# Kernel tuning notes

Hardware: AMD Instinct MI355X
Metric: run time of the kernel (lower is better)

## Reference

```python
import jax, jax.numpy as jnp
import numpy as np

B, S, HID = 4, 1024, 4096
NH, NKV, HD = 32, 8, 128
FF = 11008
EPS = 1e-6
THETA = 10000.0


def rms_norm(x, w, eps=EPS):
    v = jnp.mean(jnp.square(x), axis=-1, keepdims=True)
    return x * jax.lax.rsqrt(v + eps) * w


def rotate_half(x):
    x1, x2 = jnp.split(x, 2, axis=-1)
    return jnp.concatenate([-x2, x1], axis=-1)


def rope_cos_sin(position_ids, head_dim=HD, theta=THETA):
    inv_freq = 1.0 / (theta ** (jnp.arange(0, head_dim, 2, dtype=jnp.float32) / head_dim))
    freqs = position_ids.astype(jnp.float32)[..., None] * inv_freq  # [B,S,HD/2]
    emb = jnp.concatenate([freqs, freqs], axis=-1)  # [B,S,HD]
    return jnp.cos(emb)[:, None, :, :], jnp.sin(emb)[:, None, :, :]  # [B,1,S,HD]


def setup_inputs() -> dict:
    key = jax.random.key(0)
    ks = jax.random.split(key, 9)
    sc = 0.02
    pos = jnp.tile(jnp.arange(S, dtype=jnp.int64 if jax.config.jax_enable_x64 else jnp.int32)[None, :], (B, 1))
    causal = jnp.tril(jnp.ones((S, S), dtype=bool))
    mask = jnp.where(causal, 0.0, -1e9).astype(jnp.float32)[None, None]  # [1,1,S,S]
    return {
        "hidden_states": jax.random.normal(ks[0], (B * S, HID), jnp.float32),
        "position_ids": pos,
        "attn_mask": mask,
        "Wq": jax.random.normal(ks[1], (HID, NH * HD), jnp.float32) * sc,
        "Wk": jax.random.normal(ks[2], (HID, NKV * HD), jnp.float32) * sc,
        "Wv": jax.random.normal(ks[3], (HID, NKV * HD), jnp.float32) * sc,
        "Wo": jax.random.normal(ks[4], (NH * HD, HID), jnp.float32) * sc,
        "ln1_w": jnp.ones((HID,), jnp.float32),
        "ln2_w": jnp.ones((HID,), jnp.float32),
        "w_gate": jax.random.normal(ks[5], (HID, FF), jnp.float32) * sc,
        "w_up": jax.random.normal(ks[6], (HID, FF), jnp.float32) * sc,
        "w_down": jax.random.normal(ks[7], (FF, HID), jnp.float32) * sc,
    }


def reference(hidden_states, position_ids, attn_mask, Wq, Wk, Wv, Wo, ln1_w, ln2_w, w_gate, w_up, w_down):
    residual = hidden_states
    h = rms_norm(hidden_states, ln1_w)

    # QKV projections on flat tokens, then reshape per train partition
    q = (h @ Wq).reshape(B, S, NH, HD).transpose(0, 2, 1, 3)     # [B,NH,S,HD]
    k = (h @ Wk).reshape(B, S, NKV, HD).transpose(0, 2, 1, 3)    # [B,NKV,S,HD]
    v = (h @ Wv).reshape(B, S, NKV, HD).transpose(0, 2, 1, 3)

    cos, sin = rope_cos_sin(position_ids)
    q = q * cos + rotate_half(q) * sin
    k = k * cos + rotate_half(k) * sin

    n_rep = NH // NKV
    k = jnp.repeat(k, n_rep, axis=1)  # [B,NH,S,HD]
    v = jnp.repeat(v, n_rep, axis=1)

    scores = jnp.einsum('bhqd,bhkd->bhqk', q, k) / np.sqrt(HD)
    scores = scores + attn_mask
    # softmax in fp32 as in the source
    probs = jax.nn.softmax(scores.astype(jnp.float32), axis=-1).astype(q.dtype)
    attn = jnp.einsum('bhqk,bhkd->bhqd', probs, v)               # [B,NH,S,HD]
    attn = attn.transpose(0, 2, 1, 3).reshape(B * S, NH * HD)
    h = attn @ Wo

    h = residual + h
    residual = h
    h2 = rms_norm(h, ln2_w)
    mlp = (jax.nn.silu(h2 @ w_gate) * (h2 @ w_up)) @ w_down
    return residual + mlp
```

## Files before the change

kernel.cpp:

```cpp
#include <hip/hip_runtime.h>

#define DEVINL __device__ __forceinline__

typedef unsigned short u16;
typedef __attribute__((ext_vector_type(8))) short bf16x8;
typedef __attribute__((ext_vector_type(4))) float f32x4;
typedef __attribute__((ext_vector_type(4))) unsigned short u16x4;


DEVINL float bf2f(u16 u) { union { unsigned i; float f; } x; x.i = ((unsigned)u) << 16; return x.f; }
DEVINL u16 f2bf(float f) {
  union { float f; unsigned i; } x; x.f = f;
  unsigned r = x.i + 0x7fffu + ((x.i >> 16) & 1u);
  return (u16)(r >> 16);
}

DEVINL void async16(u16* lds, const u16* g) {
  __builtin_amdgcn_global_load_lds((const __attribute__((address_space(1))) unsigned*)g,
                                   (__attribute__((address_space(3))) unsigned*)lds, 16, 0, 0);
}

__global__ __launch_bounds__(256) void conv_t(const float* __restrict__ in,
                                              u16* __restrict__ out, int K, int N) {
  __shared__ float tile[64][65];
  int k0 = blockIdx.y << 6, n0 = blockIdx.x << 6;
  int t = threadIdx.x;
  int r = t >> 4, c4 = (t & 15) << 2;
  #pragma unroll
  for (int it = 0; it < 4; it++) {
    int row = r + it*16;
    f32x4 v = *(const f32x4*)(in + (size_t)(k0 + row)*N + n0 + c4);
    tile[row][c4+0] = v[0]; tile[row][c4+1] = v[1];
    tile[row][c4+2] = v[2]; tile[row][c4+3] = v[3];
  }
  __syncthreads();
  #pragma unroll
  for (int it = 0; it < 4; it++) {
    int nrow = r + it*16;
    u16x4 ov;
    #pragma unroll
    for (int e = 0; e < 4; e++) ov[e] = f2bf(tile[c4+e][nrow]);
    *(u16x4*)(out + (size_t)(n0 + nrow)*K + k0 + c4) = ov;
  }
}

__global__ __launch_bounds__(256) void rmsnorm_kernel(const float* __restrict__ x,
                                                      const float* __restrict__ w,
                                                      u16* __restrict__ out) {
  int row = blockIdx.x, t = threadIdx.x;
  const float* xr = x + (size_t)row * 4096;
  f32x4 v[4];
  float ss = 0.f;
  #pragma unroll
  for (int i = 0; i < 4; i++) {
    v[i] = *(const f32x4*)(xr + (t + 256*i)*4);
    ss += v[i][0]*v[i][0] + v[i][1]*v[i][1] + v[i][2]*v[i][2] + v[i][3]*v[i][3];
  }
  #pragma unroll
  for (int d = 1; d < 64; d <<= 1) ss += __shfl_xor(ss, d, 64);
  __shared__ float ps[4];
  if ((t & 63) == 0) ps[t >> 6] = ss;
  __syncthreads();
  float scale = rsqrtf((ps[0]+ps[1]+ps[2]+ps[3]) * (1.f/4096.f) + 1e-6f);
  #pragma unroll
  for (int i = 0; i < 4; i++) {
    f32x4 wv = *(const f32x4*)(w + (t + 256*i)*4);
    u16x4 o;
    #pragma unroll
    for (int e = 0; e < 4; e++) o[e] = f2bf(v[i][e] * scale * wv[e]);
    *(u16x4*)(out + (size_t)row*4096 + (t + 256*i)*4) = o;
  }
}

__global__ __launch_bounds__(256) void rope_kernel(u16* __restrict__ q, u16* __restrict__ k) {
  int tok = blockIdx.x;
  int s = tok & 1023;
  __shared__ float cs[64], sn[64];
  int t = threadIdx.x;
  if (t < 64) {
    float inv = __expf(-(float)t * 0.14391156934f);
    float ang = (float)s * inv;
    cs[t] = cosf(ang); sn[t] = sinf(ang);
  }
  __syncthreads();
  const float qscale = 0.08838834764831845f;
  size_t qbase = (size_t)tok * 4096;
  #pragma unroll
  for (int it = 0; it < 8; it++) {
    int item = t + it*256; int h = item >> 6, j = item & 63;
    size_t i0 = qbase + h*128 + j;
    float x1 = bf2f(q[i0]), x2 = bf2f(q[i0+64]);
    float c = cs[j], si = sn[j];
    q[i0]    = f2bf((x1*c - x2*si) * qscale);
    q[i0+64] = f2bf((x2*c + x1*si) * qscale);
  }
  size_t kbase = (size_t)tok * 1024;
  #pragma unroll
  for (int it = 0; it < 2; it++) {
    int item = t + it*256; int h = item >> 6, j = item & 63;
    size_t i0 = kbase + h*128 + j;
    float x1 = bf2f(k[i0]), x2 = bf2f(k[i0+64]);
    float c = cs[j], si = sn[j];
    k[i0]    = f2bf(x1*c - x2*si);
    k[i0+64] = f2bf(x2*c + x1*si);
  }
}

__global__ __launch_bounds__(256) void vtrans(const u16* __restrict__ v, u16* __restrict__ vt) {
  __shared__ u16 tile[32][33];
  int bh = blockIdx.z; int b = bh >> 3, kvh = bh & 7;
  int d0 = blockIdx.x << 5, s0 = blockIdx.y << 5;
  int tx = threadIdx.x, ty = threadIdx.y;
  for (int r = ty; r < 32; r += 8)
    tile[r][tx] = v[(size_t)(b*1024 + s0 + r)*1024 + kvh*128 + d0 + tx];
  __syncthreads();
  for (int r = ty; r < 32; r += 8)
    vt[(size_t)((b*8 + kvh)*128 + d0 + r)*1024 + s0 + tx] = tile[tx][r];
}

template<int EPI>
__global__ __launch_bounds__(256, 2) void gemm_bt(
    const u16* __restrict__ A, const u16* __restrict__ Bt,
    void* __restrict__ Cv, const float* __restrict__ resid,
    const u16* __restrict__ gate, int M, int N, int K) {
  __shared__ u16 As[128*64];
  __shared__ u16 Bs[128*64];
  int nwg = gridDim.x;
  int bid = (int)blockIdx.x;
  int cpx = nwg >> 3;
  int swz = (bid & 7) * cpx + (bid >> 3);
  int mt = M >> 7;
  int m0 = (swz % mt) << 7;
  int n0 = (swz / mt) << 7;
  int tid = threadIdx.x;
  int lane = tid & 63, wave = tid >> 6;
  int wm = wave >> 1, wn = wave & 1;

  f32x4 acc[4][4];
  f32x4 zero = {0.f, 0.f, 0.f, 0.f};
  #pragma unroll
  for (int i = 0; i < 4; i++)
    #pragma unroll
    for (int j = 0; j < 4; j++) acc[i][j] = zero;

  int arow[4], acolb[4];
  #pragma unroll
  for (int i = 0; i < 4; i++) {
    int c = i*256 + tid;
    arow[i]  = c >> 3;
    acolb[i] = ((c & 7) * 16) ^ ((arow[i] & 7) << 4);
  }

  int nsteps = K >> 6;
  for (int t = 0; t < nsteps; t++) {
    int k0 = t << 6;
    #pragma unroll
    for (int i = 0; i < 4; i++) {
      async16(As + i*2048 + wave*512, A  + (size_t)(m0 + arow[i])*K + k0 + (acolb[i] >> 1));
      async16(Bs + i*2048 + wave*512, Bt + (size_t)(n0 + arow[i])*K + k0 + (acolb[i] >> 1));
    }
    __syncthreads();
    #pragma unroll
    for (int ks = 0; ks < 2; ks++) {
      bf16x8 af[4], bfr[4];
      int c2 = (ks*32 + (lane >> 4)*8) * 2;
      #pragma unroll
      for (int mf = 0; mf < 4; mf++) {
        int r = wm*64 + mf*16 + (lane & 15);
        af[mf] = *(const bf16x8*)(As + r*64 + ((c2 ^ ((r & 7) << 4)) >> 1));
      }
      #pragma unroll
      for (int nf = 0; nf < 4; nf++) {
        int r = wn*64 + nf*16 + (lane & 15);
        bfr[nf] = *(const bf16x8*)(Bs + r*64 + ((c2 ^ ((r & 7) << 4)) >> 1));
      }
      #pragma unroll
      for (int mf = 0; mf < 4; mf++)
        #pragma unroll
        for (int nf = 0; nf < 4; nf++)
          acc[mf][nf] = __builtin_amdgcn_mfma_f32_16x16x32_bf16(af[mf], bfr[nf], acc[mf][nf], 0, 0, 0);
    }
    __syncthreads();
  }

  #pragma unroll
  for (int mf = 0; mf < 4; mf++)
    #pragma unroll
    for (int nf = 0; nf < 4; nf++)
      #pragma unroll
      for (int j = 0; j < 4; j++) {
        int rr = m0 + wm*64 + mf*16 + (lane >> 4)*4 + j;
        int cc = n0 + wn*64 + nf*16 + (lane & 15);
        size_t idx = (size_t)rr * N + cc;
        float v = acc[mf][nf][j];
        if constexpr (EPI == 0) {
          ((u16*)Cv)[idx] = f2bf(v);
        } else if constexpr (EPI == 1) {
          ((float*)Cv)[idx] = v + resid[idx];
        } else {
          float g = bf2f(gate[idx]);
          float sg = g / (1.f + __expf(-g));
          ((u16*)Cv)[idx] = f2bf(sg * v);
        }
      }
}

#define MIDBAR() do { __builtin_amdgcn_sched_barrier(0); __builtin_amdgcn_s_barrier(); \
  asm volatile("s_waitcnt lgkmcnt(0)" ::: "memory"); __builtin_amdgcn_sched_barrier(0); } while (0)
#define ENDBAR() do { __builtin_amdgcn_sched_barrier(0); __builtin_amdgcn_s_barrier(); } while (0)
#define MFMAQ(qm, qn, bq) do { \
  __builtin_amdgcn_s_setprio(1); \
  _Pragma("unroll") for (int mf_ = 0; mf_ < 4; mf_++) \
  _Pragma("unroll") for (int nf_ = 0; nf_ < 2; nf_++) \
  _Pragma("unroll") for (int ks_ = 0; ks_ < 2; ks_++) \
    acc[(qm)*4+mf_][(qn)*2+nf_] = __builtin_amdgcn_mfma_f32_16x16x32_bf16( \
        af[mf_][ks_], bq[nf_][ks_], acc[(qm)*4+mf_][(qn)*2+nf_], 0, 0, 0); \
  __builtin_amdgcn_s_setprio(0); } while (0)

template<int EPI>
__global__ __launch_bounds__(512, 2) void gemm256(
    const u16* __restrict__ A, const u16* __restrict__ Bt,
    void* __restrict__ Cv, const float* __restrict__ resid,
    const u16* __restrict__ gate, int M, int N, int K) {
  extern __shared__ u16 lds[];
  int nwg = gridDim.x, bid = (int)blockIdx.x;
  int cpx = nwg >> 3;
  int swz = (bid & 7) * cpx + (bid >> 3);
  int mt = M >> 8;
  int m0 = (swz % mt) << 8;
  int n0 = (swz / mt) << 8;
  int tid = threadIdx.x, lane = tid & 63, wave = tid >> 6;
  int wm = wave >> 2, wn = wave & 3;

  f32x4 acc[8][4];
  f32x4 zero = {0.f, 0.f, 0.f, 0.f};
  #pragma unroll
  for (int i = 0; i < 8; i++)
    #pragma unroll
    for (int j = 0; j < 4; j++) acc[i][j] = zero;

  int sgrow = lane >> 3;
  int sgcol = ((lane & 7) ^ (lane >> 3)) << 3;
  const u16* gA = A  + (size_t)(m0 + wave*8 + sgrow) * K + sgcol;
  const u16* gB = Bt + (size_t)(n0 + wave*8 + sgrow) * K + sgcol;
  size_t K64 = (size_t)64 * K, K128 = (size_t)128 * K, K192 = (size_t)192 * K;

  int rA = lane & 15;
  int sw = rA & 7;
  int acol0 = (((lane >> 4)    ) ^ sw) << 3;
  int acol1 = (((lane >> 4) + 4) ^ sw) << 3;

  bf16x8 af[4][2], b0[2][2], b1[2][2];

  auto stageA = [&](int kb, int k0) {
    u16* d = lds + kb*32768 + wave*512;
    const u16* s = gA + k0;
    async16(d,         s);
    async16(d + 4096,  s + K64);
    async16(d + 8192,  s + K128);
    async16(d + 12288, s + K192);
  };
  auto stageB = [&](int kb, int k0) {
    u16* d = lds + kb*32768 + 16384 + wave*512;
    const u16* s = gB + k0;
    async16(d,         s);
    async16(d + 4096,  s + K64);
    async16(d + 8192,  s + K128);
    async16(d + 12288, s + K192);
  };
  auto loadA = [&](int kb, int qm) {
    const u16* base = lds + kb*32768 + (wm*128 + qm*64 + rA)*64;
    #pragma unroll
    for (int mf = 0; mf < 4; mf++) {
      af[mf][0] = *(const bf16x8*)(base + mf*1024 + acol0);
      af[mf][1] = *(const bf16x8*)(base + mf*1024 + acol1);
    }
  };
  auto loadB = [&](int kb, int qn, bf16x8 (&bq)[2][2]) {
    const u16* base = lds + kb*32768 + 16384 + (wn*64 + qn*32 + rA)*64;
    #pragma unroll
    for (int nf = 0; nf < 2; nf++) {
      bq[nf][0] = *(const bf16x8*)(base + nf*1024 + acol0);
      bq[nf][1] = *(const bf16x8*)(base + nf*1024 + acol1);
    }
  };

  int nt = K >> 6;
  stageA(0, 0); stageB(0, 0);
  if (nt > 1) { stageA(1, 64); stageB(1, 64); }
  __builtin_amdgcn_sched_barrier(0);
  if (nt > 1) asm volatile("s_waitcnt vmcnt(8)" ::: "memory");
  else        asm volatile("s_waitcnt vmcnt(0)" ::: "memory");
  __builtin_amdgcn_sched_barrier(0);
  __builtin_amdgcn_s_barrier();

  for (int k = 0; k < nt; k++) {
    int kb = k & 1;
    bool pre = (k + 2) < nt;
    int k2 = (k + 2) << 6;
    loadA(kb, 0); loadB(kb, 0, b0);
    MIDBAR(); MFMAQ(0, 0, b0); ENDBAR();
    loadB(kb, 1, b1);
    MIDBAR(); MFMAQ(0, 1, b1); ENDBAR();
    loadA(kb, 1);
    if (pre) stageB(kb, k2);
    MIDBAR(); MFMAQ(1, 0, b0); ENDBAR();
    if (pre) stageA(kb, k2);
    MIDBAR(); MFMAQ(1, 1, b1);
    __builtin_amdgcn_sched_barrier(0);
    if (pre) asm volatile("s_waitcnt vmcnt(8)" ::: "memory");
    else     asm volatile("s_waitcnt vmcnt(0)" ::: "memory");
    __builtin_amdgcn_sched_barrier(0);
    __builtin_amdgcn_s_barrier();
  }

  #pragma unroll
  for (int mf = 0; mf < 8; mf++)
    #pragma unroll
    for (int nf = 0; nf < 4; nf++)
      #pragma unroll
      for (int j = 0; j < 4; j++) {
        int rr = m0 + wm*128 + mf*16 + (lane >> 4)*4 + j;
        int cc = n0 + wn*64 + nf*16 + (lane & 15);
        size_t idx = (size_t)rr * N + cc;
        float v = acc[mf][nf][j];
        if constexpr (EPI == 0) {
          ((u16*)Cv)[idx] = f2bf(v);
        } else if constexpr (EPI == 1) {
          ((float*)Cv)[idx] = v + resid[idx];
        } else {
          float g = bf2f(gate[idx]);
          float sg = g / (1.f + __expf(-g));
          ((u16*)Cv)[idx] = f2bf(sg * v);
        }
      }
}

__global__ __launch_bounds__(256, 2) void attn_kernel(
    const u16* __restrict__ q, const u16* __restrict__ k,
    const u16* __restrict__ vt, u16* __restrict__ out) {
  __shared__ u16 Ks[64*128];
  __shared__ u16 Vs[128*64];
  __shared__ u16 Ps[4*16*64];
  int bid = blockIdx.x;
  int qt = bid & 15;
  int h  = (bid >> 4) & 31;
  int b  = bid >> 9;
  int kvh = h >> 2;
  int tid = threadIdx.x, lane = tid & 63, wave = tid >> 6;
  int q0 = qt << 6;

  bf16x8 qf[4];
  {
    const u16* qb_ = q + (size_t)(b*1024 + q0 + wave*16 + (lane & 15))*4096 + h*128 + (lane >> 4)*8;
    #pragma unroll
    for (int ks = 0; ks < 4; ks++) qf[ks] = *(const bf16x8*)(qb_ + ks*32);
  }
  f32x4 o[8];
  f32x4 zero = {0.f,0.f,0.f,0.f};
  #pragma unroll
  for (int i = 0; i < 8; i++) o[i] = zero;
  float m[4] = {-1e30f,-1e30f,-1e30f,-1e30f};
  float l[4] = {0.f,0.f,0.f,0.f};

  int kr[4], kc[4], vr[4], vc[4];
  #pragma unroll
  for (int i = 0; i < 4; i++) {
    int c = i*256 + tid;
    kr[i] = c >> 4; kc[i] = ((c & 15)*16) ^ ((kr[i] & 7) << 4);
    vr[i] = c >> 3; vc[i] = ((c & 7)*16)  ^ ((vr[i] & 7) << 4);
  }

  for (int t = 0; t <= qt; t++) {
    int kv0 = t << 6;
    #pragma unroll
    for (int i = 0; i < 4; i++) {
      async16(Ks + i*2048 + wave*512, k  + (size_t)(b*1024 + kv0 + kr[i])*1024 + kvh*128 + (kc[i] >> 1));
      async16(Vs + i*2048 + wave*512, vt + (size_t)((b*8 + kvh)*128 + vr[i])*1024 + kv0 + (vc[i] >> 1));
    }
    __syncthreads();

    f32x4 s[4];
    #pragma unroll
    for (int nf = 0; nf < 4; nf++) {
      s[nf] = zero;
      #pragma unroll
      for (int ks = 0; ks < 4; ks++) {
        int r = nf*16 + (lane & 15);
        int c2 = (ks*32 + (lane >> 4)*8)*2;
        bf16x8 kf = *(const bf16x8*)(Ks + r*128 + ((c2 ^ ((r & 7) << 4)) >> 1));
        s[nf] = __builtin_amdgcn_mfma_f32_16x16x32_bf16(qf[ks], kf, s[nf], 0, 0, 0);
      }
    }
    if (t == qt) {
      #pragma unroll
      for (int nf = 0; nf < 4; nf++)
        #pragma unroll
        for (int j = 0; j < 4; j++) {
          int cc = nf*16 + (lane & 15);
          int rr = wave*16 + (lane >> 4)*4 + j;
          if (cc > rr) s[nf][j] = -1e30f;
        }
    }
    #pragma unroll
    for (int j = 0; j < 4; j++) {
      float mx = fmaxf(fmaxf(s[0][j], s[1][j]), fmaxf(s[2][j], s[3][j]));
      #pragma unroll
      for (int d = 1; d < 16; d <<= 1) mx = fmaxf(mx, __shfl_xor(mx, d, 64));
      float mn = fmaxf(m[j], mx);
      float f = __expf(m[j] - mn);
      m[j] = mn;
      float ssum = 0.f;
      #pragma unroll
      for (int nf = 0; nf < 4; nf++) {
        float p = __expf(s[nf][j] - mn);
        s[nf][j] = p; ssum += p;
      }
      #pragma unroll
      for (int d = 1; d < 16; d <<= 1) ssum += __shfl_xor(ssum, d, 64);
      l[j] = l[j]*f + ssum;
      #pragma unroll
      for (int nf = 0; nf < 8; nf++) o[nf][j] *= f;
    }
    #pragma unroll
    for (int nf = 0; nf < 4; nf++)
      #pragma unroll
      for (int j = 0; j < 4; j++) {
        int rr = (lane >> 4)*4 + j;
        int cb = ((nf*16 + (lane & 15))*2) ^ ((rr & 7) << 4);
        Ps[wave*1024 + rr*64 + (cb >> 1)] = f2bf(s[nf][j]);
      }
    #pragma unroll
    for (int ks2 = 0; ks2 < 2; ks2++) {
      int mr = lane & 15;
      int c2 = (ks2*32 + (lane >> 4)*8)*2;
      bf16x8 pa = *(const bf16x8*)(Ps + wave*1024 + mr*64 + ((c2 ^ ((mr & 7) << 4)) >> 1));
      #pragma unroll
      for (int nf = 0; nf < 8; nf++) {
        int d = nf*16 + (lane & 15);
        bf16x8 vf = *(const bf16x8*)(Vs + d*64 + ((c2 ^ ((d & 7) << 4)) >> 1));
        o[nf] = __builtin_amdgcn_mfma_f32_16x16x32_bf16(pa, vf, o[nf], 0, 0, 0);
      }
    }
    __syncthreads();
  }

  float inv[4];
  #pragma unroll
  for (int j = 0; j < 4; j++) inv[j] = 1.f / l[j];
  u16* ob = out + (size_t)(b*1024 + q0 + wave*16)*4096 + h*128;
  #pragma unroll
  for (int nf = 0; nf < 8; nf++)
    #pragma unroll
    for (int j = 0; j < 4; j++) {
      int rr = (lane >> 4)*4 + j;
      int cc = nf*16 + (lane & 15);
      ob[(size_t)rr*4096 + cc] = f2bf(o[nf][j] * inv[j]);
    }
}

extern "C" void kernel_launch(void* const* d_in, const int* in_sizes, int n_in,
                              void* d_out, int out_size, void* d_ws, size_t ws_size,
                              hipStream_t stream) {
  (void)in_sizes; (void)n_in; (void)out_size;
  const float* hidden = (const float*)d_in[0];
  const float* Wq  = (const float*)d_in[3];
  const float* Wk  = (const float*)d_in[4];
  const float* Wv  = (const float*)d_in[5];
  const float* Wo  = (const float*)d_in[6];
  const float* ln1 = (const float*)d_in[7];
  const float* ln2 = (const float*)d_in[8];
  const float* Wg  = (const float*)d_in[9];
  const float* Wu  = (const float*)d_in[10];
  const float* Wd  = (const float*)d_in[11];
  float* out = (float*)d_out;

  char* ws = (char*)d_ws;
  size_t off = 0;
  auto alloc = [&](size_t b) { char* p = ws + off; off += (b + 4095) & ~(size_t)4095; return p; };
  u16*  W1   = (u16*)alloc(90177536);
  u16*  h1   = (u16*)alloc(33554432);
  u16*  qb   = (u16*)alloc(33554432);
  u16*  kb   = (u16*)alloc(8388608);
  u16*  vb   = (u16*)alloc(8388608);
  u16*  vtb  = (u16*)alloc(8388608);
  float* hmid = (float*)alloc(67108864);
  u16*  gb   = (u16*)alloc(90177536);
  if (off > ws_size) return;

  u16* wqT = W1;
  u16* wkT = W1 + 16777216;
  u16* wvT = wkT + 4194304;

  hipFuncSetAttribute((const void*)gemm256<0>, hipFuncAttributeMaxDynamicSharedMemorySize, 131072);
  hipFuncSetAttribute((const void*)gemm256<1>, hipFuncAttributeMaxDynamicSharedMemorySize, 131072);
  hipFuncSetAttribute((const void*)gemm256<2>, hipFuncAttributeMaxDynamicSharedMemorySize, 131072);

  dim3 blk(256);
  conv_t<<<dim3(64, 64),  blk, 0, stream>>>(Wq, wqT, 4096, 4096);
  conv_t<<<dim3(16, 64),  blk, 0, stream>>>(Wk, wkT, 4096, 1024);
  conv_t<<<dim3(16, 64),  blk, 0, stream>>>(Wv, wvT, 4096, 1024);
  rmsnorm_kernel<<<4096, blk, 0, stream>>>(hidden, ln1, h1);
  gemm256<0><<<256, 512, 131072, stream>>>(h1, wqT, qb, nullptr, nullptr, 4096, 4096, 4096);
  gemm_bt<0><<<256, blk, 0, stream>>>(h1, wkT, kb, nullptr, nullptr, 4096, 1024, 4096);
  gemm_bt<0><<<256, blk, 0, stream>>>(h1, wvT, vb, nullptr, nullptr, 4096, 1024, 4096);
  rope_kernel<<<4096, blk, 0, stream>>>(qb, kb);
  vtrans<<<dim3(4, 32, 32), dim3(32, 8), 0, stream>>>(vb, vtb);
  attn_kernel<<<2048, blk, 0, stream>>>(qb, kb, vtb, h1);
  conv_t<<<dim3(64, 64), blk, 0, stream>>>(Wo, W1, 4096, 4096);
  gemm256<1><<<256, 512, 131072, stream>>>(h1, W1, hmid, hidden, nullptr, 4096, 4096, 4096);
  rmsnorm_kernel<<<4096, blk, 0, stream>>>(hmid, ln2, qb);
  conv_t<<<dim3(172, 64), blk, 0, stream>>>(Wg, W1, 4096, 11008);
  gemm256<0><<<688, 512, 131072, stream>>>(qb, W1, gb, nullptr, nullptr, 4096, 11008, 4096);
  conv_t<<<dim3(172, 64), blk, 0, stream>>>(Wu, W1, 4096, 11008);
  gemm256<2><<<688, 512, 131072, stream>>>(qb, W1, gb, nullptr, gb, 4096, 11008, 4096);
  conv_t<<<dim3(64, 172), blk, 0, stream>>>(Wd, W1, 11008, 4096);
  gemm256<1><<<256, 512, 131072, stream>>>(gb, W1, out, hmid, nullptr, 4096, 4096, 11008);
}
```

Before: 1.864 ms.

## Cut GEMM main-loop barriers from eight to two per K step

Restructures the 256x256 bf16 GEMM inner loop. All B fragments and the first A half are loaded up front, then two MFMA quadrants are issued back to back. A single LDS wait and barrier sits before the prefetch of the next stage, and the old four-phase interleave with barriers around every quadrant is gone. This is meant to cut barrier stalls and give the compiler larger MFMA blocks. In exchange, LDS reads and MFMAs overlap less finely across waves, and register pressure may rise.

```diff
diff --git a/kernel.cpp b/kernel.cpp
--- a/kernel.cpp
+++ b/kernel.cpp
@@ -205,17 +205,14 @@
       }
 }
 
-#define MIDBAR() do { __builtin_amdgcn_sched_barrier(0); __builtin_amdgcn_s_barrier(); \
-  asm volatile("s_waitcnt lgkmcnt(0)" ::: "memory"); __builtin_amdgcn_sched_barrier(0); } while (0)
-#define ENDBAR() do { __builtin_amdgcn_sched_barrier(0); __builtin_amdgcn_s_barrier(); } while (0)
-#define MFMAQ(qm, qn, bq) do { \
-  __builtin_amdgcn_s_setprio(1); \
+#define SB0() __builtin_amdgcn_sched_barrier(0)
+#define MFMAQ2(qm, qn, afr, bq) do { \
   _Pragma("unroll") for (int mf_ = 0; mf_ < 4; mf_++) \
   _Pragma("unroll") for (int nf_ = 0; nf_ < 2; nf_++) \
   _Pragma("unroll") for (int ks_ = 0; ks_ < 2; ks_++) \
     acc[(qm)*4+mf_][(qn)*2+nf_] = __builtin_amdgcn_mfma_f32_16x16x32_bf16( \
-        af[mf_][ks_], bq[nf_][ks_], acc[(qm)*4+mf_][(qn)*2+nf_], 0, 0, 0); \
-  __builtin_amdgcn_s_setprio(0); } while (0)
+        afr[mf_][ks_], bq[nf_][ks_], acc[(qm)*4+mf_][(qn)*2+nf_], 0, 0, 0); \
+} while (0)
 
 template<int EPI>
 __global__ __launch_bounds__(512, 2) void gemm256(
@@ -288,29 +285,37 @@
   int nt = K >> 6;
   stageA(0, 0); stageB(0, 0);
   if (nt > 1) { stageA(1, 64); stageB(1, 64); }
-  __builtin_amdgcn_sched_barrier(0);
+  SB0();
   if (nt > 1) asm volatile("s_waitcnt vmcnt(8)" ::: "memory");
   else        asm volatile("s_waitcnt vmcnt(0)" ::: "memory");
-  __builtin_amdgcn_sched_barrier(0);
+  SB0();
   __builtin_amdgcn_s_barrier();
 
   for (int k = 0; k < nt; k++) {
     int kb = k & 1;
     bool pre = (k + 2) < nt;
     int k2 = (k + 2) << 6;
-    loadA(kb, 0); loadB(kb, 0, b0);
-    MIDBAR(); MFMAQ(0, 0, b0); ENDBAR();
-    loadB(kb, 1, b1);
-    MIDBAR(); MFMAQ(0, 1, b1); ENDBAR();
+    loadA(kb, 0); loadB(kb, 0, b0); loadB(kb, 1, b1);
+    SB0();
+    __builtin_amdgcn_s_setprio(1);
+    MFMAQ2(0, 0, af, b0);
+    MFMAQ2(0, 1, af, b1);
+    __builtin_amdgcn_s_setprio(0);
     loadA(kb, 1);
-    if (pre) stageB(kb, k2);
-    MIDBAR(); MFMAQ(1, 0, b0); ENDBAR();
-    if (pre) stageA(kb, k2);
-    MIDBAR(); MFMAQ(1, 1, b1);
-    __builtin_amdgcn_sched_barrier(0);
+    SB0();
+    asm volatile("s_waitcnt lgkmcnt(0)" ::: "memory");
+    SB0();
+    __builtin_amdgcn_s_barrier();
+    if (pre) { stageB(kb, k2); stageA(kb, k2); }
+    SB0();
+    __builtin_amdgcn_s_setprio(1);
+    MFMAQ2(1, 0, af, b0);
+    MFMAQ2(1, 1, af, b1);
+    __builtin_amdgcn_s_setprio(0);
+    SB0();
     if (pre) asm volatile("s_waitcnt vmcnt(8)" ::: "memory");
     else     asm volatile("s_waitcnt vmcnt(0)" ::: "memory");
-    __builtin_amdgcn_sched_barrier(0);
+    SB0();
     __builtin_amdgcn_s_barrier();
   }
 
```

Result: faster. 1.811 ms (-2.9%).
